# Performance work log

Hardware: AMD Instinct MI355X
Metric: run time of the kernel (lower is better)

The kernel has to match this reference:

```python
import jax, jax.numpy as jnp
import numpy as np

NUM_SAMPLES = 32
B, H, W = 4, 400, 400
NEAR, FAR = 2.0, 6.0


def setup_inputs() -> dict:
    key = jax.random.key(0)
    k1, k2 = jax.random.split(key)
    predictions = jax.random.normal(k1, (B, H, W, NUM_SAMPLES, 4), dtype=jnp.float32)
    # sorted sample depths along each ray in [NEAR, FAR]
    u = jax.random.uniform(k2, (B, H, W, NUM_SAMPLES), dtype=jnp.float32)
    t_vals = jnp.sort(NEAR + (FAR - NEAR) * u, axis=-1)
    return {"predictions": predictions, "t_vals": t_vals}


def reference(predictions, t_vals):
    # predictions: [B,H,W,N,4], t_vals: [B,H,W,N]
    rgb = jax.nn.sigmoid(predictions[..., :3])          # [B,H,W,N,3]
    sigma = jax.nn.relu(predictions[..., 3])            # [B,H,W,N]
    delta = t_vals[..., 1:] - t_vals[..., :-1]
    big = jnp.full(t_vals.shape[:-1] + (1,), 1e10, dtype=t_vals.dtype)
    delta = jnp.concatenate([delta, big], axis=-1)      # [B,H,W,N]
    alpha = 1.0 - jnp.exp(-sigma * delta)
    exp_term = 1.0 - alpha
    # exclusive cumprod along sample axis
    cp = jnp.cumprod(exp_term + 1e-10, axis=-1)
    transmittance = jnp.concatenate(
        [jnp.ones_like(cp[..., :1]), cp[..., :-1]], axis=-1)
    weights = alpha * transmittance                     # [B,H,W,N]
    rgb_map = jnp.sum(weights[..., None] * rgb, axis=-2)   # [B,H,W,3]
    depth_map = jnp.sum(weights * t_vals, axis=-1)          # [B,H,W]
    return rgb_map, depth_map
```

## Files before the change

### kernel.cpp

```cpp
#include <hip/hip_runtime.h>


__global__ __launch_bounds__(256) void nerf_render_kernel(
    const float4* __restrict__ pred4,
    const float*  __restrict__ tvals,
    float* __restrict__ out_rgb,
    float* __restrict__ out_depth,
    int total_samples)
{
    const int gid = blockIdx.x * 256 + threadIdx.x;
    if (gid >= total_samples) return;
    const int lane = threadIdx.x & 31;
    const int ray  = gid >> 5;

    const float4 p  = pred4[gid];
    const float  tv = tvals[gid];

    const float tn    = __shfl_down(tv, 1, 32);
    const float delta = (lane == 31) ? 1e10f : (tn - tv);

    const float sigma = fmaxf(p.w, 0.0f);
    const float et    = __expf(-sigma * delta);
    const float alpha = 1.0f - et;
    const float ep    = et + 1e-10f;

    float v = ep;
    #pragma unroll
    for (int off = 1; off < 32; off <<= 1) {
        const float t = __shfl_up(v, off, 32);
        v = (lane >= off) ? v * t : v;
    }
    float T = __shfl_up(v, 1, 32);
    T = (lane == 0) ? 1.0f : T;

    const float w = alpha * T;
    float r = w / (1.0f + __expf(-p.x));
    float g = w / (1.0f + __expf(-p.y));
    float b = w / (1.0f + __expf(-p.z));
    float d = w * tv;

    #pragma unroll
    for (int off = 16; off >= 1; off >>= 1) {
        r += __shfl_down(r, off, 32);
        g += __shfl_down(g, off, 32);
        b += __shfl_down(b, off, 32);
        d += __shfl_down(d, off, 32);
    }

    if (lane == 0) {
        out_rgb[ray * 3 + 0] = r;
        out_rgb[ray * 3 + 1] = g;
        out_rgb[ray * 3 + 2] = b;
        out_depth[ray]       = d;
    }
}

extern "C" void kernel_launch(void* const* d_in, const int* in_sizes, int n_in,
                              void* d_out, int out_size, void* d_ws, size_t ws_size,
                              hipStream_t stream) {
    const float4* pred4 = (const float4*)d_in[0];
    const float*  tvals = (const float*)d_in[1];

    const int total_samples = in_sizes[1];
    const int rays          = total_samples / 32;

    float* out_rgb   = (float*)d_out;
    float* out_depth = (float*)d_out + (size_t)rays * 3;

    const int block = 256;
    const int grid  = (total_samples + block - 1) / block;
    nerf_render_kernel<<<grid, block, 0, stream>>>(pred4, tvals, out_rgb,
                                                   out_depth, total_samples);
}
```

Measured before the change: 465.0 us.

## Map one thread per ray with sequential transmittance scan instead of wave shuffles

Replaces the one-thread-per-sample layout, which used wave shuffles for the prefix product and the reduction, with one thread per ray. Each thread loads its 32 depth values as float4 and walks the samples in order, keeping transmittance and the rgb/depth sums in registers. This removes the shuffle scan and reduction, and it also swaps the divides for hardware reciprocals. In exchange, each thread makes strided 512-byte loads that coalesce poorly across the wave, uses more registers, and launches far fewer threads.

```diff
diff --git a/kernel.cpp b/kernel.cpp
--- a/kernel.cpp
+++ b/kernel.cpp
@@ -1,65 +1,62 @@
 #include <hip/hip_runtime.h>
 
 
-__global__ __launch_bounds__(256) void nerf_render_kernel(
+__global__ __launch_bounds__(256) void nerf_ray_kernel(
     const float4* __restrict__ pred4,
-    const float*  __restrict__ tvals,
+    const float4* __restrict__ t4,
     float* __restrict__ out_rgb,
     float* __restrict__ out_depth,
-    int total_samples)
+    int rays)
 {
-    const int gid = blockIdx.x * 256 + threadIdx.x;
-    if (gid >= total_samples) return;
-    const int lane = threadIdx.x & 31;
-    const int ray  = gid >> 5;
+    const int ray = blockIdx.x * 256 + threadIdx.x;
+    if (ray >= rays) return;
 
-    const float4 p  = pred4[gid];
-    const float  tv = tvals[gid];
+    float tt[33];
+    {
+        const float4* tp = t4 + (size_t)ray * 8;
+        #pragma unroll
+        for (int k = 0; k < 8; ++k) {
+            const float4 q = tp[k];
+            tt[4*k+0] = q.x; tt[4*k+1] = q.y; tt[4*k+2] = q.z; tt[4*k+3] = q.w;
+        }
+        tt[32] = tt[31] + 1e10f;
+    }
 
-    const float tn    = __shfl_down(tv, 1, 32);
-    const float delta = (lane == 31) ? 1e10f : (tn - tv);
-
-    const float sigma = fmaxf(p.w, 0.0f);
-    const float et    = __expf(-sigma * delta);
-    const float alpha = 1.0f - et;
-    const float ep    = et + 1e-10f;
-
-    float v = ep;
-    #pragma unroll
-    for (int off = 1; off < 32; off <<= 1) {
-        const float t = __shfl_up(v, off, 32);
-        v = (lane >= off) ? v * t : v;
-    }
-    float T = __shfl_up(v, 1, 32);
-    T = (lane == 0) ? 1.0f : T;
-
-    const float w = alpha * T;
-    float r = w / (1.0f + __expf(-p.x));
-    float g = w / (1.0f + __expf(-p.y));
-    float b = w / (1.0f + __expf(-p.z));
-    float d = w * tv;
+    float T = 1.0f, r = 0.0f, g = 0.0f, b = 0.0f, d = 0.0f;
+    const float4* pp = pred4 + (size_t)ray * 32;
 
     #pragma unroll
-    for (int off = 16; off >= 1; off >>= 1) {
-        r += __shfl_down(r, off, 32);
-        g += __shfl_down(g, off, 32);
-        b += __shfl_down(b, off, 32);
-        d += __shfl_down(d, off, 32);
+    for (int c = 0; c < 4; ++c) {
+        float4 P[8];
+        #pragma unroll
+        for (int k = 0; k < 8; ++k) P[k] = pp[c * 8 + k];
+
+        #pragma unroll
+        for (int k = 0; k < 8; ++k) {
+            const int   j     = c * 8 + k;
+            const float delta = tt[j + 1] - tt[j];
+            const float sg    = fmaxf(P[k].w, 0.0f);
+            const float et    = __expf(-sg * delta);
+            const float w     = T * (1.0f - et);
+            r += w * __builtin_amdgcn_rcpf(1.0f + __expf(-P[k].x));
+            g += w * __builtin_amdgcn_rcpf(1.0f + __expf(-P[k].y));
+            b += w * __builtin_amdgcn_rcpf(1.0f + __expf(-P[k].z));
+            d += w * tt[j];
+            T *= (et + 1e-10f);
+        }
     }
 
-    if (lane == 0) {
-        out_rgb[ray * 3 + 0] = r;
-        out_rgb[ray * 3 + 1] = g;
-        out_rgb[ray * 3 + 2] = b;
-        out_depth[ray]       = d;
-    }
+    out_rgb[ray * 3 + 0] = r;
+    out_rgb[ray * 3 + 1] = g;
+    out_rgb[ray * 3 + 2] = b;
+    out_depth[ray]       = d;
 }
 
 extern "C" void kernel_launch(void* const* d_in, const int* in_sizes, int n_in,
                               void* d_out, int out_size, void* d_ws, size_t ws_size,
                               hipStream_t stream) {
     const float4* pred4 = (const float4*)d_in[0];
-    const float*  tvals = (const float*)d_in[1];
+    const float4* t4    = (const float4*)d_in[1];
 
     const int total_samples = in_sizes[1];
     const int rays          = total_samples / 32;
@@ -68,7 +65,7 @@
     float* out_depth = (float*)d_out + (size_t)rays * 3;
 
     const int block = 256;
-    const int grid  = (total_samples + block - 1) / block;
-    nerf_render_kernel<<<grid, block, 0, stream>>>(pred4, tvals, out_rgb,
-                                                   out_depth, total_samples);
+    const int grid  = (rays + block - 1) / block;
+    nerf_ray_kernel<<<grid, block, 0, stream>>>(pred4, t4, out_rgb,
+                                                out_depth, rays);
 }
```

New measurement: 495.9 us. +6.7%, slower.
